# Optimization experiments

Measured on AMD Instinct MI355X. Metric: run time of the kernel, lower is better.

The kernel has to match this reference:

```python
import jax, jax.numpy as jnp
import numpy as np

N_EMB = 4096
EMB_DIM = 256
BETA = 0.25


def setup_inputs() -> dict:
    key = jax.random.key(0)
    k1, k2 = jax.random.split(key)
    z = jax.random.normal(k1, (32, EMB_DIM, 32, 32), dtype=jnp.float32)
    # nn.Embedding weight initialized uniform(-1/n_emb, 1/n_emb)
    embedding = jax.random.uniform(
        k2, (N_EMB, EMB_DIM), dtype=jnp.float32,
        minval=-1.0 / N_EMB, maxval=1.0 / N_EMB)
    return {"z": z, "embedding": embedding}


def reference(z, embedding):
    sg = jax.lax.stop_gradient
    # (B,C,H,W) -> (B,H,W,C)
    zp = jnp.transpose(z, (0, 2, 3, 1))
    zf = zp.reshape(-1, EMB_DIM)  # [N, D]
    # squared distances: ||z||^2 + ||e||^2 - 2 z e^T  -> [N, n_emb]
    d = (jnp.sum(zf * zf, axis=1, keepdims=True)
         + jnp.sum(embedding * embedding, axis=1)
         - 2.0 * jnp.matmul(zf, embedding.T))
    idx = jnp.argmin(d, axis=1)  # [N]
    min_encodings = jax.nn.one_hot(idx, N_EMB, dtype=zf.dtype)  # [N, n_emb]
    e_mean = jnp.mean(min_encodings, axis=0)
    perplexity = jnp.exp(-jnp.sum(e_mean * jnp.log(e_mean + 1e-10)))
    # gather codebook rows (same math as one-hot matmul)
    z_q = jnp.take(embedding, idx, axis=0).reshape(zp.shape)
    # straight-through estimator
    z_q_st = zp + sg(z_q - zp)
    q_latent_loss = jnp.mean((z_q_st - sg(zp)) ** 2)
    e_latent_loss = jnp.mean((sg(z_q_st) - zp) ** 2)
    loss = q_latent_loss + BETA * e_latent_loss
    z_q_out = jnp.transpose(z_q_st, (0, 3, 1, 2))  # (B,C,H,W)
    return (loss, z_q_out, perplexity, min_encodings, idx[:, None])
```

## Files before the change

### kernel.cpp

```cpp
#include <hip/hip_runtime.h>

#define N_ROWS 32768
#define NEMB   4096
#define DIM    256

#define O_LOSS 0
#define O_ZQ   1ull
#define O_PERP 8388609ull
#define O_ENC  8388610ull
#define O_IDX  142606338ull
#define Z4_BEG 2097153
#define Z4_END 35651584

#define CAP    32
#define EPS    1e-3f

typedef unsigned long long u64;
typedef __attribute__((ext_vector_type(8))) __bf16 bf16x8;
typedef __attribute__((ext_vector_type(4))) float  f32x4;


__device__ __forceinline__ unsigned int f2bf1(float x) {
    unsigned int u = __float_as_uint(x);
    return (u + 0x7fffu + ((u >> 16) & 1u)) >> 16;
}
__device__ __forceinline__ unsigned int f2bf2(float lo, float hi) {
    return f2bf1(lo) | (f2bf1(hi) << 16);
}

__global__ __launch_bounds__(256)
void vq_prep(const float* __restrict__ z, const float* __restrict__ emb,
             unsigned short* __restrict__ zbf, unsigned short* __restrict__ embsw,
             int* __restrict__ counts, float* __restrict__ out)
{
    const int tid = threadIdx.x, blk = blockIdx.x;
    if (blk < 1024) {
        __shared__ float L[32][256];
        const int b = blk >> 5, sub = blk & 31;
        const int c0 = (sub >> 2) << 5;
        const int hw0 = (sub & 3) << 8;
        const float* zp = z + (size_t)b * 262144 + hw0 + tid;
#pragma unroll 8
        for (int i = 0; i < 32; ++i)
            L[i][tid] = zp[(size_t)(c0 + i) << 10];
        __syncthreads();
        const int n = (b << 10) + hw0 + tid;
        unsigned int pk[16];
#pragma unroll
        for (int c2 = 0; c2 < 16; ++c2)
            pk[c2] = f2bf2(L[2 * c2][tid], L[2 * c2 + 1][tid]);
        uint4* dst = (uint4*)((char*)zbf + (size_t)n * 512 + (size_t)c0 * 2);
#pragma unroll
        for (int q = 0; q < 4; ++q)
            dst[q] = make_uint4(pk[4*q], pk[4*q+1], pk[4*q+2], pk[4*q+3]);
    } else {
        const int base = ((blk - 1024) << 8) + tid;
#pragma unroll
        for (int q = 0; q < 4; ++q) {
            const int ch = (base << 2) + q;
            const int code = ch >> 5, cw = ch & 31;
            const float* ep = emb + (size_t)code * 256 + cw * 8;
            float4 e0 = *(const float4*)ep;
            float4 e1 = *(const float4*)(ep + 4);
            uint4 pk = make_uint4(f2bf2(e0.x, e0.y), f2bf2(e0.z, e0.w),
                                  f2bf2(e1.x, e1.y), f2bf2(e1.z, e1.w));
            *(uint4*)((char*)embsw + (size_t)code * 512 + (size_t)((cw ^ (code & 7)) << 4)) = pk;
        }
        if (blk == 1024) {
            for (int j = tid; j < NEMB; j += 256) counts[j] = 0;
            if (tid == 0) {
                out[O_ENC] = 0.f; out[O_ENC + 1] = 0.f;
                out[(size_t)Z4_END * 4] = 0.f; out[(size_t)Z4_END * 4 + 1] = 0.f;
            }
        }
    }
}

__global__ __launch_bounds__(512, 2)
void vq_filter(const float* __restrict__ z, const float* __restrict__ emb,
               const unsigned short* __restrict__ zbf_us,
               const unsigned short* __restrict__ embsw,
               float* __restrict__ out, u64* __restrict__ ws_best)
{
#pragma clang fp contract(off)
    __shared__ __align__(16) char Bsh[65536];
    __shared__ float zsumS[256];
    __shared__ float rowmaxS[256];
    __shared__ unsigned short rowlist[256][CAP];
    __shared__ int rowcnt[256];
    __shared__ int nflag;
    __shared__ int flagrows[32];
    __shared__ u64 flagbest[32];

    const int tid = threadIdx.x;
    const int blk = blockIdx.x;
    const int rb  = blk >> 1;
    const int hv  = blk & 1;
    const int n0  = rb << 8;
    const int C0  = hv << 11;
    const int b   = n0 >> 10;
    const int hw0 = n0 & 1023;
    const int w    = tid >> 6;
    const int lane = tid & 63;
    const int r0w  = w << 5;
    const int arow = lane & 15;
    const int akg  = lane >> 4;
    const float* zb = z + (size_t)b * 262144 + hw0;

    if (tid < 32) flagbest[tid] = ~0ull;
    if (tid == 0) nflag = 0;

    if (tid < 256) {
        rowcnt[tid] = 0;
        const float* gz = zb + tid;
        float hs0, hs1;
        {
            float r[8];
#pragma unroll
            for (int j = 0; j < 8; ++j) { float v = gz[(size_t)j << 10]; r[j] = v * v; }
            for (int m = 1; m < 16; ++m)
#pragma unroll
                for (int j = 0; j < 8; ++j) {
                    float v = gz[(size_t)(8 * m + j) << 10];
                    float sq = v * v;
                    r[j] = r[j] + sq;
                }
            hs0 = ((r[0] + r[1]) + (r[2] + r[3])) + ((r[4] + r[5]) + (r[6] + r[7]));
        }
        {
            float r[8];
#pragma unroll
            for (int j = 0; j < 8; ++j) { float v = gz[(size_t)(128 + j) << 10]; r[j] = v * v; }
            for (int m = 1; m < 16; ++m)
#pragma unroll
                for (int j = 0; j < 8; ++j) {
                    float v = gz[(size_t)(128 + 8 * m + j) << 10];
                    float sq = v * v;
                    r[j] = r[j] + sq;
                }
            hs1 = ((r[0] + r[1]) + (r[2] + r[3])) + ((r[4] + r[5]) + (r[6] + r[7]));
        }
        zsumS[tid] = hs0 + hs1;
    }

    bf16x8 A[2][8];
#pragma unroll
    for (int rf = 0; rf < 2; ++rf)
#pragma unroll
        for (int s = 0; s < 8; ++s)
            A[rf][s] = *(const bf16x8*)((const char*)zbf_us
                        + ((size_t)(n0 + r0w + rf * 16 + arow) << 9)
                        + (size_t)((s * 32 + akg * 8) << 1));

    auto stage = [&](int buf, int ct) {
        const char* sb = (const char*)embsw + (((size_t)(C0 + (ct << 6))) << 9)
                         + (w << 10) + (lane << 4);
        char* db = Bsh + buf * 32768 + (w << 10);
#pragma unroll
        for (int it = 0; it < 4; ++it) {
            __builtin_amdgcn_global_load_lds(
                (const __attribute__((address_space(1))) unsigned int*)(sb + it * 8192),
                (__attribute__((address_space(3))) unsigned int*)(db + it * 8192),
                16, 0, 0);
        }
    };

    float vmax[2][4];
#pragma unroll
    for (int rf = 0; rf < 2; ++rf)
#pragma unroll
        for (int j = 0; j < 4; ++j) vmax[rf][j] = -3.4e38f;
    float thr[2][4];

    const size_t zf_base = (size_t)Z4_BEG + (size_t)blk * 131072;

    for (int pass = 0; pass < 2; ++pass) {
        stage(0, 0);
        __syncthreads();
        for (int ct = 0; ct < 32; ++ct) {
            const int buf = ct & 1;
            if (ct < 31) stage(buf ^ 1, ct + 1);

            {
                const int iter = pass * 32 + ct;
                const size_t g = zf_base + (size_t)iter * 2048 + tid;
                const float4 zv = make_float4(0.f, 0.f, 0.f, 0.f);
#pragma unroll
                for (int q = 0; q < 4; ++q) {
                    const size_t i4 = g + (size_t)q * 512;
                    if (i4 < (size_t)Z4_END) ((float4*)out)[i4] = zv;
                }
            }

            f32x4 acc[2][4];
            const f32x4 zz = {0.f, 0.f, 0.f, 0.f};
#pragma unroll
            for (int rf = 0; rf < 2; ++rf)
#pragma unroll
                for (int cf = 0; cf < 4; ++cf) acc[rf][cf] = zz;

            const char* bufp = Bsh + buf * 32768;
#pragma unroll
            for (int s = 0; s < 8; ++s) {
#pragma unroll
                for (int cf = 0; cf < 4; ++cf) {
                    const int cl = (cf << 4) + arow;
                    const int off = (cl << 9) + (((s << 6) + (akg << 4)) ^ ((cl & 7) << 4));
                    bf16x8 bb = *(const bf16x8*)(bufp + off);
                    acc[0][cf] = __builtin_amdgcn_mfma_f32_16x16x32_bf16(A[0][s], bb, acc[0][cf], 0, 0, 0);
                    acc[1][cf] = __builtin_amdgcn_mfma_f32_16x16x32_bf16(A[1][s], bb, acc[1][cf], 0, 0, 0);
                }
            }

            if (pass == 0) {
#pragma unroll
                for (int rf = 0; rf < 2; ++rf)
#pragma unroll
                    for (int cf = 0; cf < 4; ++cf)
#pragma unroll
                        for (int j = 0; j < 4; ++j)
                            vmax[rf][j] = fmaxf(vmax[rf][j], acc[rf][cf][j]);
            } else {
#pragma unroll
                for (int rf = 0; rf < 2; ++rf)
#pragma unroll
                    for (int cf = 0; cf < 4; ++cf)
#pragma unroll
                        for (int j = 0; j < 4; ++j) {
                            const float v = acc[rf][cf][j];
                            if (v >= thr[rf][j]) {
                                const int row  = r0w + rf * 16 + akg * 4 + j;
                                const int code = (ct << 6) + (cf << 4) + arow;
                                const int slot = atomicAdd(&rowcnt[row], 1);
                                if (slot < CAP) rowlist[row][slot] = (unsigned short)code;
                                else if (slot == CAP) {
                                    const int fi = atomicAdd(&nflag, 1);
                                    if (fi < 32) flagrows[fi] = row;
                                }
                            }
                        }
            }
            __syncthreads();
        }
        if (pass == 0) {
#pragma unroll
            for (int rf = 0; rf < 2; ++rf)
#pragma unroll
                for (int j = 0; j < 4; ++j) {
                    float v = vmax[rf][j];
                    v = fmaxf(v, __shfl_xor(v, 1));
                    v = fmaxf(v, __shfl_xor(v, 2));
                    v = fmaxf(v, __shfl_xor(v, 4));
                    v = fmaxf(v, __shfl_xor(v, 8));
                    vmax[rf][j] = v;
                }
            if ((lane & 15) == 0) {
#pragma unroll
                for (int rf = 0; rf < 2; ++rf)
#pragma unroll
                    for (int j = 0; j < 4; ++j)
                        rowmaxS[r0w + rf * 16 + akg * 4 + j] = vmax[rf][j];
            }
            __syncthreads();
#pragma unroll
            for (int rf = 0; rf < 2; ++rf)
#pragma unroll
                for (int j = 0; j < 4; ++j)
                    thr[rf][j] = rowmaxS[r0w + rf * 16 + akg * 4 + j] - EPS;
        }
    }
    __syncthreads();

    if (tid < 256) {
        const int cnt = rowcnt[tid];
        if (cnt <= CAP) {
            const float zs = zsumS[tid];
            const float* zrow = zb + tid;
            u64 bestk = ~0ull;
            for (int basec = 0; basec < cnt; basec += 8) {
                int codes[8];
#pragma unroll
                for (int j = 0; j < 8; ++j) {
                    const int jj = basec + j;
                    codes[j] = rowlist[tid][jj < cnt ? jj : basec];
                }
                const float* ep[8];
#pragma unroll
                for (int j = 0; j < 8; ++j) ep[j] = emb + ((size_t)(C0 + codes[j]) << 8);
                float a8[8] = {0.f, 0.f, 0.f, 0.f, 0.f, 0.f, 0.f, 0.f};
#pragma unroll 2
                for (int k4 = 0; k4 < 64; ++k4) {
                    const float zv0 = zrow[(size_t)(4 * k4 + 0) << 10];
                    const float zv1 = zrow[(size_t)(4 * k4 + 1) << 10];
                    const float zv2 = zrow[(size_t)(4 * k4 + 2) << 10];
                    const float zv3 = zrow[(size_t)(4 * k4 + 3) << 10];
                    float4 e4[8];
#pragma unroll
                    for (int j = 0; j < 8; ++j) e4[j] = *(const float4*)(ep[j] + 4 * k4);
#pragma unroll
                    for (int j = 0; j < 8; ++j) {
                        a8[j] = fmaf(zv0, e4[j].x, a8[j]);
                        a8[j] = fmaf(zv1, e4[j].y, a8[j]);
                        a8[j] = fmaf(zv2, e4[j].z, a8[j]);
                        a8[j] = fmaf(zv3, e4[j].w, a8[j]);
                    }
                }
#pragma unroll
                for (int j = 0; j < 8; ++j) {
                    if (basec + j < cnt) {
                        const float d = fmaf(-2.f, a8[j], zs);
                        const u64 key = ((u64)__float_as_uint(d) << 32)
                                      | (unsigned)(C0 + codes[j]);
                        if (key < bestk) bestk = key;
                    }
                }
            }
            ws_best[((size_t)(n0 + tid) << 1) + hv] = bestk;
        }
    }
    __syncthreads();

    const int nf = (nflag > 32) ? 32 : nflag;
    for (int f = 0; f < nf; ++f) {
        const int fr = flagrows[f];
        if (tid < 256) {
            const float zs = zsumS[fr];
            const float* zrow = zb + fr;
            const float* ep0 = emb + ((size_t)(C0 + (tid << 3)) << 8);
            float a8[8] = {0.f, 0.f, 0.f, 0.f, 0.f, 0.f, 0.f, 0.f};
#pragma unroll 2
            for (int k4 = 0; k4 < 64; ++k4) {
                const float zv0 = zrow[(size_t)(4 * k4 + 0) << 10];
                const float zv1 = zrow[(size_t)(4 * k4 + 1) << 10];
                const float zv2 = zrow[(size_t)(4 * k4 + 2) << 10];
                const float zv3 = zrow[(size_t)(4 * k4 + 3) << 10];
#pragma unroll
                for (int j = 0; j < 8; ++j) {
                    const float4 e4 = *(const float4*)(ep0 + (size_t)j * 256 + 4 * k4);
                    a8[j] = fmaf(zv0, e4.x, a8[j]);
                    a8[j] = fmaf(zv1, e4.y, a8[j]);
                    a8[j] = fmaf(zv2, e4.z, a8[j]);
                    a8[j] = fmaf(zv3, e4.w, a8[j]);
                }
            }
            u64 bk = ~0ull;
#pragma unroll
            for (int j = 0; j < 8; ++j) {
                const float d = fmaf(-2.f, a8[j], zs);
                const u64 key = ((u64)__float_as_uint(d) << 32)
                              | (unsigned)(C0 + (tid << 3) + j);
                if (key < bk) bk = key;
            }
            atomicMin(&flagbest[f], bk);
        }
    }
    __syncthreads();
    if (tid < nf) ws_best[((size_t)(n0 + flagrows[tid]) << 1) + hv] = flagbest[tid];
}

__global__ void vq_scatter(const u64* __restrict__ ws_best, float* __restrict__ out,
                           int* __restrict__ counts, int* __restrict__ ws_idx)
{
    int i = blockIdx.x * 256 + threadIdx.x;
    if (i < N_ROWS) {
        u64 m = ws_best[(size_t)i * 2];
        u64 v = ws_best[(size_t)i * 2 + 1];
        if (v < m) m = v;
        int id = (int)(m & 0xffffffffu);
        ws_idx[i] = id;
        out[O_IDX + i] = (float)id;
        out[O_ENC + (size_t)i * 4096 + id] = 1.0f;
        atomicAdd(&counts[id], 1);
    }
}

__global__ __launch_bounds__(256)
void vq_zq(const float* __restrict__ z, const float* __restrict__ emb,
           const int* __restrict__ ws_idx, float* __restrict__ out,
           double* __restrict__ parts)
{
#pragma clang fp contract(off)
    __shared__ float embT[32][257];
    __shared__ int idxS[32];
    __shared__ double red[256];

    const int tid = threadIdx.x;
    const int blk = blockIdx.x;
    const int b   = blk >> 5;
    const int hw0 = (blk & 31) << 5;
    const int n0  = (b << 10) + hw0;

    if (tid < 32) idxS[tid] = ws_idx[n0 + tid];
    __syncthreads();

    {
        const int g = tid >> 3, l8 = tid & 7;
        const float* er = emb + (size_t)idxS[g] * 256;
#pragma unroll
        for (int it = 0; it < 8; ++it) {
            const float4 v = *(const float4*)(er + it * 32 + l8 * 4);
            const int c = it * 32 + l8 * 4;
            embT[g][c]     = v.x;
            embT[g][c + 1] = v.y;
            embT[g][c + 2] = v.z;
            embT[g][c + 3] = v.w;
        }
    }
    __syncthreads();

    const int r  = tid & 31;
    const int cq = tid >> 5;
    const size_t base = (size_t)b * 262144 + hw0 + r;
    double val = 0.0;
#pragma unroll 4
    for (int i = 0; i < 32; ++i) {
        const int c = i * 8 + cq;
        const size_t gid = base + (size_t)c * 1024;
        const float zp = z[gid];
        const float e  = embT[r][c];
        const float t  = e - zp;
        const float zq = zp + t;
        __builtin_nontemporal_store(zq, &out[O_ZQ + gid]);
        const float diff = zq - zp;
        val += (double)(diff * diff);
    }

    red[tid] = val;
    __syncthreads();
    for (int st = 128; st > 0; st >>= 1) {
        if (tid < st) red[tid] += red[tid + st];
        __syncthreads();
    }
    if (tid == 0) parts[blk] = red[0];
}

__global__ void vq_final(const int* __restrict__ counts,
                         const double* __restrict__ parts, float* __restrict__ out)
{
    __shared__ double red[256];
    const int t = threadIdx.x;

    double loc = 0.0;
    for (int j = t; j < NEMB; j += 256) {
        float em = (float)counts[j] * (1.0f / 32768.0f);
        float lt = em + 1e-10f;
        float lg = logf(lt);
        float pr = em * lg;
        loc += (double)pr;
    }
    red[t] = loc;
    __syncthreads();
    for (int st = 128; st > 0; st >>= 1) {
        if (t < st) red[t] += red[t + st];
        __syncthreads();
    }
    double s = red[0];
    __syncthreads();

    double q = 0.0;
    for (int j = t; j < 1024; j += 256) q += parts[j];
    red[t] = q;
    __syncthreads();
    for (int st = 128; st > 0; st >>= 1) {
        if (t < st) red[t] += red[t + st];
        __syncthreads();
    }
    if (t == 0) {
        out[O_PERP] = expf(-(float)s);
        double qm = red[0] * (1.0 / 8388608.0);
        float  qf = (float)qm;
        out[O_LOSS] = qf + 0.25f * qf;
    }
}

extern "C" void kernel_launch(void* const* d_in, const int* in_sizes, int n_in,
                              void* d_out, int out_size, void* d_ws, size_t ws_size,
                              hipStream_t stream)
{
    const float* z   = (const float*)d_in[0];
    const float* emb = (const float*)d_in[1];
    float* out = (float*)d_out;

    u64*    ws_best = (u64*)d_ws;
    int*    counts  = (int*)((char*)d_ws + 1048576);
    double* parts   = (double*)((char*)d_ws + 1064960);
    int*    ws_idx  = (int*)((char*)d_ws + 1081344);

    unsigned short* zbf   = (unsigned short*)((char*)d_out + 16);
    unsigned short* embsw = (unsigned short*)((char*)d_out + 16 + 16777216);

    vq_prep   <<<1152, 256, 0, stream>>>(z, emb, zbf, embsw, counts, out);
    vq_filter <<<256,  512, 0, stream>>>(z, emb, zbf, embsw, out, ws_best);
    vq_scatter<<<128,  256, 0, stream>>>(ws_best, out, counts, ws_idx);
    vq_zq     <<<1024, 256, 0, stream>>>(z, emb, ws_idx, out, parts);
    vq_final  <<<1,    256, 0, stream>>>(counts, parts, out);
}
```

Measured before the change: 953.1 us.

## Fuse two-pass max/filter into single pass with running-max threshold

Replaces the two GEMM passes over the codebook (the first finds each row's max score, the second collects candidates within EPS of it) with a single pass. That pass keeps a per-row running max, reduced across lanes for every tile, and appends any code within EPS of the current running max. This halves the MFMA work and the codebook staging traffic in the filter kernel, and the zero-fill stores are spread over the 32 remaining iterations. In exchange, early tiles judged against a lower running max can admit extra candidates. That raises the risk of CAP overflow and more rows falling back to the flagged-row path, and adds shuffle reductions to every tile.

```diff
diff --git a/kernel.cpp b/kernel.cpp
--- a/kernel.cpp
+++ b/kernel.cpp
@@ -85,7 +85,6 @@
 #pragma clang fp contract(off)
     __shared__ __align__(16) char Bsh[65536];
     __shared__ float zsumS[256];
-    __shared__ float rowmaxS[256];
     __shared__ unsigned short rowlist[256][CAP];
     __shared__ int rowcnt[256];
     __shared__ int nflag;
@@ -165,109 +164,80 @@
         }
     };
 
-    float vmax[2][4];
+    float runmax[2][4];
 #pragma unroll
     for (int rf = 0; rf < 2; ++rf)
 #pragma unroll
-        for (int j = 0; j < 4; ++j) vmax[rf][j] = -3.4e38f;
-    float thr[2][4];
+        for (int j = 0; j < 4; ++j) runmax[rf][j] = -3.4e38f;
 
     const size_t zf_base = (size_t)Z4_BEG + (size_t)blk * 131072;
 
-    for (int pass = 0; pass < 2; ++pass) {
-        stage(0, 0);
+    stage(0, 0);
+    __syncthreads();
+
+    for (int ct = 0; ct < 32; ++ct) {
+        const int buf = ct & 1;
+        if (ct < 31) stage(buf ^ 1, ct + 1);
+
+        {
+            const size_t g = zf_base + (size_t)ct * 4096 + tid;
+            const float4 zv = make_float4(0.f, 0.f, 0.f, 0.f);
+#pragma unroll
+            for (int q = 0; q < 8; ++q) {
+                const size_t i4 = g + (size_t)q * 512;
+                if (i4 < (size_t)Z4_END) ((float4*)out)[i4] = zv;
+            }
+        }
+
+        f32x4 acc[2][4];
+        const f32x4 zz = {0.f, 0.f, 0.f, 0.f};
+#pragma unroll
+        for (int rf = 0; rf < 2; ++rf)
+#pragma unroll
+            for (int cf = 0; cf < 4; ++cf) acc[rf][cf] = zz;
+
+        const char* bufp = Bsh + buf * 32768;
+#pragma unroll
+        for (int s = 0; s < 8; ++s) {
+#pragma unroll
+            for (int cf = 0; cf < 4; ++cf) {
+                const int cl = (cf << 4) + arow;
+                const int off = (cl << 9) + (((s << 6) + (akg << 4)) ^ ((cl & 7) << 4));
+                bf16x8 bb = *(const bf16x8*)(bufp + off);
+                acc[0][cf] = __builtin_amdgcn_mfma_f32_16x16x32_bf16(A[0][s], bb, acc[0][cf], 0, 0, 0);
+                acc[1][cf] = __builtin_amdgcn_mfma_f32_16x16x32_bf16(A[1][s], bb, acc[1][cf], 0, 0, 0);
+            }
+        }
+
+#pragma unroll
+        for (int rf = 0; rf < 2; ++rf) {
+#pragma unroll
+            for (int j = 0; j < 4; ++j) {
+                float m = fmaxf(fmaxf(acc[rf][0][j], acc[rf][1][j]),
+                                fmaxf(acc[rf][2][j], acc[rf][3][j]));
+                m = fmaxf(m, __shfl_xor(m, 1));
+                m = fmaxf(m, __shfl_xor(m, 2));
+                m = fmaxf(m, __shfl_xor(m, 4));
+                m = fmaxf(m, __shfl_xor(m, 8));
+                const float rm = fmaxf(runmax[rf][j], m);
+                runmax[rf][j] = rm;
+                const float th = rm - EPS;
+#pragma unroll
+                for (int cf = 0; cf < 4; ++cf) {
+                    if (acc[rf][cf][j] >= th) {
+                        const int row  = r0w + rf * 16 + akg * 4 + j;
+                        const int code = (ct << 6) + (cf << 4) + arow;
+                        const int slot = atomicAdd(&rowcnt[row], 1);
+                        if (slot < CAP) rowlist[row][slot] = (unsigned short)code;
+                        else if (slot == CAP) {
+                            const int fi = atomicAdd(&nflag, 1);
+                            if (fi < 32) flagrows[fi] = row;
+                        }
+                    }
+                }
+            }
+        }
         __syncthreads();
-        for (int ct = 0; ct < 32; ++ct) {
-            const int buf = ct & 1;
-            if (ct < 31) stage(buf ^ 1, ct + 1);
-
-            {
-                const int iter = pass * 32 + ct;
-                const size_t g = zf_base + (size_t)iter * 2048 + tid;
-                const float4 zv = make_float4(0.f, 0.f, 0.f, 0.f);
-#pragma unroll
-                for (int q = 0; q < 4; ++q) {
-                    const size_t i4 = g + (size_t)q * 512;
-                    if (i4 < (size_t)Z4_END) ((float4*)out)[i4] = zv;
-                }
-            }
-
-            f32x4 acc[2][4];
-            const f32x4 zz = {0.f, 0.f, 0.f, 0.f};
-#pragma unroll
-            for (int rf = 0; rf < 2; ++rf)
-#pragma unroll
-                for (int cf = 0; cf < 4; ++cf) acc[rf][cf] = zz;
-
-            const char* bufp = Bsh + buf * 32768;
-#pragma unroll
-            for (int s = 0; s < 8; ++s) {
-#pragma unroll
-                for (int cf = 0; cf < 4; ++cf) {
-                    const int cl = (cf << 4) + arow;
-                    const int off = (cl << 9) + (((s << 6) + (akg << 4)) ^ ((cl & 7) << 4));
-                    bf16x8 bb = *(const bf16x8*)(bufp + off);
-                    acc[0][cf] = __builtin_amdgcn_mfma_f32_16x16x32_bf16(A[0][s], bb, acc[0][cf], 0, 0, 0);
-                    acc[1][cf] = __builtin_amdgcn_mfma_f32_16x16x32_bf16(A[1][s], bb, acc[1][cf], 0, 0, 0);
-                }
-            }
-
-            if (pass == 0) {
-#pragma unroll
-                for (int rf = 0; rf < 2; ++rf)
-#pragma unroll
-                    for (int cf = 0; cf < 4; ++cf)
-#pragma unroll
-                        for (int j = 0; j < 4; ++j)
-                            vmax[rf][j] = fmaxf(vmax[rf][j], acc[rf][cf][j]);
-            } else {
-#pragma unroll
-                for (int rf = 0; rf < 2; ++rf)
-#pragma unroll
-                    for (int cf = 0; cf < 4; ++cf)
-#pragma unroll
-                        for (int j = 0; j < 4; ++j) {
-                            const float v = acc[rf][cf][j];
-                            if (v >= thr[rf][j]) {
-                                const int row  = r0w + rf * 16 + akg * 4 + j;
-                                const int code = (ct << 6) + (cf << 4) + arow;
-                                const int slot = atomicAdd(&rowcnt[row], 1);
-                                if (slot < CAP) rowlist[row][slot] = (unsigned short)code;
-                                else if (slot == CAP) {
-                                    const int fi = atomicAdd(&nflag, 1);
-                                    if (fi < 32) flagrows[fi] = row;
-                                }
-                            }
-                        }
-            }
-            __syncthreads();
-        }
-        if (pass == 0) {
-#pragma unroll
-            for (int rf = 0; rf < 2; ++rf)
-#pragma unroll
-                for (int j = 0; j < 4; ++j) {
-                    float v = vmax[rf][j];
-                    v = fmaxf(v, __shfl_xor(v, 1));
-                    v = fmaxf(v, __shfl_xor(v, 2));
-                    v = fmaxf(v, __shfl_xor(v, 4));
-                    v = fmaxf(v, __shfl_xor(v, 8));
-                    vmax[rf][j] = v;
-                }
-            if ((lane & 15) == 0) {
-#pragma unroll
-                for (int rf = 0; rf < 2; ++rf)
-#pragma unroll
-                    for (int j = 0; j < 4; ++j)
-                        rowmaxS[r0w + rf * 16 + akg * 4 + j] = vmax[rf][j];
-            }
-            __syncthreads();
-#pragma unroll
-            for (int rf = 0; rf < 2; ++rf)
-#pragma unroll
-                for (int j = 0; j < 4; ++j)
-                    thr[rf][j] = rowmaxS[r0w + rf * 16 + akg * 4 + j] - EPS;
-        }
     }
     __syncthreads();
 
```

After: 1.411 ms. 1.48x slower.
